# Performance work log

Hardware: AMD Instinct MI355X
Metric: run time of the kernel (lower is better)

The kernel has to match this reference:

```python
import jax, jax.numpy as jnp
import numpy as np

B, S, D, H = 2, 2048, 1024, 16
DQ = D // H
EPS = 1e-5


def setup_inputs() -> dict:
    key = jax.random.key(0)
    ks = jax.random.split(key, 6)
    scale = 0.02
    return {
        "x": jax.random.normal(ks[0], (B, S, D), dtype=jnp.float32),
        "ln_g": jnp.ones((D,), dtype=jnp.float32),
        "ln_b": jnp.zeros((D,), dtype=jnp.float32),
        "Wq": jax.random.normal(ks[1], (D, D), dtype=jnp.float32) * scale,
        "bq": jnp.zeros((D,), dtype=jnp.float32),
        "Wk": jax.random.normal(ks[2], (D, D), dtype=jnp.float32) * scale,
        "bk": jnp.zeros((D,), dtype=jnp.float32),
        "Wv": jax.random.normal(ks[3], (D, D), dtype=jnp.float32) * scale,
        "bv": jnp.zeros((D,), dtype=jnp.float32),
        "Wo": jax.random.normal(ks[4], (D, D), dtype=jnp.float32) * scale,
        "bo": jnp.zeros((D,), dtype=jnp.float32),
    }


def reference(x, ln_g, ln_b, Wq, bq, Wk, bk, Wv, bv, Wo, bo):
    # pre-LayerNorm (torch default eps=1e-5, biased variance)
    mu = jnp.mean(x, axis=-1, keepdims=True)
    var = jnp.mean((x - mu) ** 2, axis=-1, keepdims=True)
    xn = (x - mu) * jax.lax.rsqrt(var + EPS) * ln_g + ln_b

    # QKV projections; weights stored [d_in, d_out]
    q = xn @ Wq + bq  # [B,S,D]
    k = xn @ Wk + bk
    v = xn @ Wv + bv

    # split heads -> [B,H,S,DQ]
    def heads(t):
        return t.reshape(B, S, H, DQ).transpose(0, 2, 1, 3)
    q, k, v = heads(q), heads(k), heads(v)

    scores = jnp.einsum("bhqd,bhkd->bhqk", q, k) / jnp.sqrt(jnp.float32(DQ))
    causal = jnp.tril(jnp.ones((S, S), dtype=bool))  # True = keep
    scores = jnp.where(causal, scores, -jnp.inf)
    probs = jax.nn.softmax(scores, axis=-1)
    attn = jnp.einsum("bhqk,bhkd->bhqd", probs, v)  # [B,H,S,DQ]

    # merge heads: [B,H,S,DQ] -> [B,S,H*DQ] (matches transpose/flatten/transpose)
    merged = attn.transpose(0, 2, 1, 3).reshape(B, S, D)
    out = merged @ Wo + bo
    return out + x
```

## Files before the change

### kernel.cpp

```cpp
#include <hip/hip_runtime.h>
#include <math.h>

#define BB 2
#define SS 2048
#define DD 1024
#define HH 16
#define DQK 64
#define NROWS (BB * SS)
#define NE ((size_t)BB * SS * DD)

using short8 = __attribute__((ext_vector_type(8))) short;
using f32x4  = __attribute__((ext_vector_type(4))) float;

__device__ __forceinline__ ushort f2bf(float f) {
  union { float f; unsigned u; } c; c.f = f;
  return (ushort)((c.u + 0x7fffu + ((c.u >> 16) & 1u)) >> 16);
}

__device__ __forceinline__ unsigned cvt_pk_bf16(float lo, float hi) {
  unsigned r;
  asm("v_cvt_pk_bf16_f32 %0, %1, %2" : "=v"(r) : "v"(lo), "v"(hi));
  return r;
}

__device__ __forceinline__ f32x4 mfma16(short8 a, short8 b, f32x4 c) {
  return __builtin_amdgcn_mfma_f32_16x16x32_bf16(a, b, c, 0, 0, 0);
}

typedef __attribute__((address_space(1))) const unsigned gas_u32;
typedef __attribute__((address_space(3))) unsigned las_u32;
__device__ __forceinline__ void gload_lds16(const void* g, void* l) {
  __builtin_amdgcn_global_load_lds((gas_u32*)g, (las_u32*)l, 16, 0, 0);
}

__global__ __launch_bounds__(256) void prep(const float* __restrict__ x,
                                            const float* __restrict__ g,
                                            const float* __restrict__ bta,
                                            ushort* __restrict__ xn,
                                            const float* __restrict__ Wq,
                                            const float* __restrict__ Wk,
                                            const float* __restrict__ Wv,
                                            const float* __restrict__ Wo,
                                            ushort* __restrict__ wt) {
  __shared__ float tile[64][65];
  const int t = threadIdx.x;
  if (blockIdx.x < NROWS) {
    const int row = blockIdx.x;
    float4 v = ((const float4*)(x + (size_t)row * DD))[t];
    float s  = v.x + v.y + v.z + v.w;
    float ss = v.x * v.x + v.y * v.y + v.z * v.z + v.w * v.w;
#pragma unroll
    for (int off = 32; off > 0; off >>= 1) {
      s  += __shfl_xor(s, off);
      ss += __shfl_xor(ss, off);
    }
    const int wid = t >> 6, lane = t & 63;
    if (lane == 0) { tile[0][wid] = s; tile[0][4 + wid] = ss; }
    __syncthreads();
    const float stot  = tile[0][0] + tile[0][1] + tile[0][2] + tile[0][3];
    const float sstot = tile[0][4] + tile[0][5] + tile[0][6] + tile[0][7];
    const float mu  = stot * (1.0f / DD);
    const float var = sstot * (1.0f / DD) - mu * mu;
    const float inv = rsqrtf(var + 1e-5f);
    const float4 g4 = ((const float4*)g)[t];
    const float4 b4 = ((const float4*)bta)[t];
    ushort4 o;
    o.x = f2bf((v.x - mu) * inv * g4.x + b4.x);
    o.y = f2bf((v.y - mu) * inv * g4.y + b4.y);
    o.z = f2bf((v.z - mu) * inv * g4.z + b4.z);
    o.w = f2bf((v.w - mu) * inv * g4.w + b4.w);
    ((ushort4*)(xn + (size_t)row * DD))[t] = o;
  } else {
    const int wb = blockIdx.x - NROWS;
    const int z = wb >> 8;
    const int k0 = (wb & 15) * 64, n0 = ((wb >> 4) & 15) * 64;
    const float* W = (z == 0) ? Wq : (z == 1) ? Wk : (z == 2) ? Wv : Wo;
    ushort* dst = wt + (size_t)z * DD * DD;
    const int tr = t >> 4, tc = (t & 15) * 4;
#pragma unroll
    for (int rr = 0; rr < 64; rr += 16) {
      float4 v = *(const float4*)(W + (size_t)(k0 + rr + tr) * DD + n0 + tc);
      tile[rr + tr][tc + 0] = v.x;
      tile[rr + tr][tc + 1] = v.y;
      tile[rr + tr][tc + 2] = v.z;
      tile[rr + tr][tc + 3] = v.w;
    }
    __syncthreads();
#pragma unroll
    for (int rr = 0; rr < 64; rr += 16) {
      const int n = rr + tr;
      ushort4 o;
      o.x = f2bf(tile[tc + 0][n]);
      o.y = f2bf(tile[tc + 1][n]);
      o.z = f2bf(tile[tc + 2][n]);
      o.w = f2bf(tile[tc + 3][n]);
      *(ushort4*)(dst + (size_t)(n0 + n) * DD + k0 + tc) = o;
    }
  }
}

#define GEMM_CORE(Ag, Bg)                                                     \
  f32x4 acc[4][4];                                                            \
  _Pragma("unroll")                                                           \
  for (int m = 0; m < 4; ++m)                                                 \
    _Pragma("unroll")                                                         \
    for (int n = 0; n < 4; ++n) acc[m][n] = (f32x4){0.f, 0.f, 0.f, 0.f};     \
  const int cs = ((t & 3) * 16) ^ (((t >> 3) & 3) * 16);                      \
  const int fsw = ((r16 >> 1) & 3) * 16;                                      \
  {                                                                           \
    GSTAGE(Ag, Bg, 0, 0);                                                     \
    GSTAGE(Ag, Bg, 1, 32);                                                    \
    int cb = 0;                                                               \
    for (int k0 = 0; k0 < DD; k0 += 32) {                                     \
      __builtin_amdgcn_sched_barrier(0);                                      \
      if (k0 + 32 < DD) {                                                     \
        asm volatile("s_waitcnt vmcnt(4)" ::: "memory");                      \
      } else {                                                                \
        asm volatile("s_waitcnt vmcnt(0)" ::: "memory");                      \
      }                                                                       \
      __builtin_amdgcn_s_barrier();                                           \
      __builtin_amdgcn_sched_barrier(0);                                      \
      if (k0 + 64 < DD) {                                                     \
        int nb = cb + 2; if (nb >= 3) nb -= 3;                                \
        GSTAGE(Ag, Bg, nb, k0 + 64);                                          \
      }                                                                       \
      const char* Ac = (const char*)&As[cb][0][0];                            \
      const char* Bc = (const char*)&Bs[cb][0][0];                            \
      short8 af[4], bf[4];                                                    \
      _Pragma("unroll")                                                       \
      for (int m = 0; m < 4; ++m)                                             \
        af[m] = *(const short8*)(Ac + (wr * 64 + m * 16 + r16) * 64 +         \
                                 ((g * 16) ^ fsw));                           \
      _Pragma("unroll")                                                       \
      for (int n = 0; n < 4; ++n)                                             \
        bf[n] = *(const short8*)(Bc + (wc * 64 + n * 16 + r16) * 64 +         \
                                 ((g * 16) ^ fsw));                           \
      _Pragma("unroll")                                                       \
      for (int m = 0; m < 4; ++m)                                             \
        _Pragma("unroll")                                                     \
        for (int n = 0; n < 4; ++n) acc[m][n] = mfma16(af[m], bf[n], acc[m][n]); \
      cb = (cb + 1 == 3) ? 0 : cb + 1;                                        \
    }                                                                         \
  }

#define GSTAGE(Ag, Bg, buf, k0)                                               \
  {                                                                           \
    _Pragma("unroll")                                                         \
    for (int i = 0; i < 2; ++i) {                                             \
      gload_lds16(Ag + (size_t)(row0 + i * 64 + (t >> 2)) * (DD * 2) +        \
                      (k0) * 2 + cs,                                          \
                  (char*)&As[buf][0][0] + i * 4096 + t * 16);                 \
      gload_lds16(Bg + (size_t)(col0 + i * 64 + (t >> 2)) * (DD * 2) +        \
                      (k0) * 2 + cs,                                          \
                  (char*)&Bs[buf][0][0] + i * 4096 + t * 16);                 \
    }                                                                         \
  }

__global__ __launch_bounds__(256) void gemm_qkv(
    const ushort* __restrict__ A, const ushort* __restrict__ wt,
    const float* __restrict__ bq, const float* __restrict__ bk,
    const float* __restrict__ bv, ushort* __restrict__ qb,
    ushort* __restrict__ kb, ushort* __restrict__ vt) {
  __shared__ ushort As[3][128][32];
  __shared__ ushort Bs[3][128][32];
  const int t = threadIdx.x;
  const int lane = t & 63;
  const int w = t >> 6, wr = w >> 1, wc = w & 1;
  const int r16 = lane & 15, g = lane >> 4;
  const int row0 = blockIdx.x * 128;
  const int mat = blockIdx.y >> 3;
  const int col0 = (blockIdx.y & 7) * 128;
  const char* Ag = (const char*)A;
  const char* Bg = (const char*)(wt + (size_t)mat * DD * DD);
  const float* bias = (mat == 0) ? bq : (mat == 1) ? bk : bv;
  const float scl = (mat == 0) ? 0.125f * 1.44269504f : 1.0f;

  GEMM_CORE(Ag, Bg)

#pragma unroll
  for (int n = 0; n < 4; ++n) {
    const int c = col0 + wc * 64 + n * 16 + r16;
    const float bc = bias[c];
#pragma unroll
    for (int m = 0; m < 4; ++m) {
      const int rbase = row0 + wr * 64 + m * 16 + g * 4;
      if (mat < 2) {
        ushort* outb = (mat == 0) ? qb : kb;
#pragma unroll
        for (int e = 0; e < 4; ++e)
          outb[(size_t)(rbase + e) * DD + c] = f2bf((acc[m][n][e] + bc) * scl);
      } else {
        uint2 st;
        st.x = cvt_pk_bf16(acc[m][n][0] + bc, acc[m][n][1] + bc);
        st.y = cvt_pk_bf16(acc[m][n][2] + bc, acc[m][n][3] + bc);
        const size_t vrow = (size_t)((rbase >> 11) * HH + (c >> 6)) * DQK + (c & 63);
        *(uint2*)(vt + vrow * SS + (rbase & 2047)) = st;
      }
    }
  }
}

__global__ __launch_bounds__(256) void gemm_o(
    const ushort* __restrict__ A, const ushort* __restrict__ Bt,
    const float* __restrict__ bias, const float* __restrict__ resid,
    float* __restrict__ outf) {
  __shared__ ushort As[3][128][32];
  __shared__ ushort Bs[3][128][32];
  const int t = threadIdx.x;
  const int lane = t & 63;
  const int w = t >> 6, wr = w >> 1, wc = w & 1;
  const int r16 = lane & 15, g = lane >> 4;
  const int row0 = blockIdx.x * 128;
  const int col0 = blockIdx.y * 128;
  const char* Ag = (const char*)A;
  const char* Bg = (const char*)Bt;

  GEMM_CORE(Ag, Bg)

#pragma unroll
  for (int n = 0; n < 4; ++n) {
    const int c = col0 + wc * 64 + n * 16 + r16;
    const float bc = bias[c];
#pragma unroll
    for (int m = 0; m < 4; ++m) {
      const int rbase = row0 + wr * 64 + m * 16 + g * 4;
#pragma unroll
      for (int e = 0; e < 4; ++e) {
        const size_t idx = (size_t)(rbase + e) * DD + c;
        outf[idx] = acc[m][n][e] + bc + resid[idx];
      }
    }
  }
}

__global__ __launch_bounds__(256) void attn_mfma(const ushort* __restrict__ Q,
                                                 const ushort* __restrict__ K,
                                                 const ushort* __restrict__ Vt,
                                                 ushort* __restrict__ O) {
  __shared__ ushort Ks[2][64][64];
  __shared__ ushort Vs[2][64][64];

  const int t = threadIdx.x, lane = t & 63, ww = t >> 6;
  const int r16 = lane & 15, g = lane >> 4;

  const int bid = blockIdx.x;
  const int xcd = bid & 7;
  const int bh = xcd * 4 + ((bid >> 3) & 3);
  const int m = (bid >> 5) & 7;
  const int j = bid >> 8;
  const int qb = (j == 0) ? (31 - m) : (j == 1) ? m : (j == 2) ? (23 - m) : (8 + m);
  const int b = bh >> 4, h = bh & 15;
  const size_t tokbase = (size_t)b * SS;
  const size_t hoff = (size_t)h * DQK;
  const int q0 = qb * 64 + ww * 16;
  const int nt = qb + 1;

  const int srow = t >> 3;
  const int scol = (t & 7) * 16;
  const char* Kb = (const char*)(K + tokbase * DD + hoff);
  const char* Vb = (const char*)(Vt + (size_t)bh * DQK * SS);
  const int sw = ((r16 & 3) | ((r16 >> 1) & 4)) << 4;
  const int rlo = (r16 & 3) + ((r16 >> 2) << 3);

#define STAGE(buf, j0)                                                        \
  {                                                                           \
    _Pragma("unroll")                                                         \
    for (int i = 0; i < 2; ++i) {                                             \
      const int R = i * 32 + srow;                                            \
      const int Cs = scol ^ (((R & 3) | ((R >> 1) & 4)) << 4);                \
      gload_lds16(Kb + ((size_t)((j0) + R) * DD) * 2 + Cs,                    \
                  (char*)&Ks[buf][0][0] + i * 4096 + ww * 1024);              \
      gload_lds16(Vb + ((size_t)R * SS + (j0)) * 2 + Cs,                      \
                  (char*)&Vs[buf][0][0] + i * 4096 + ww * 1024);              \
    }                                                                         \
  }

  short8 qf[2];
#pragma unroll
  for (int kc = 0; kc < 2; ++kc)
    qf[kc] = *(const short8*)(Q + (tokbase + q0 + r16) * DD + hoff + kc * 32 + g * 8);

  f32x4 o[4];
#pragma unroll
  for (int dt = 0; dt < 4; ++dt) o[dt] = (f32x4){0.f, 0.f, 0.f, 0.f};
  float rm = -INFINITY, rl = 0.f;

  STAGE(0, 0);
  int cur = 0;
  for (int tt = 0; tt < nt; ++tt) {
    __builtin_amdgcn_sched_barrier(0);
    asm volatile("s_waitcnt vmcnt(0)" ::: "memory");
    __builtin_amdgcn_s_barrier();
    __builtin_amdgcn_sched_barrier(0);
    if (tt + 1 < nt) STAGE(cur ^ 1, (tt + 1) * 64);

    const char* Kc = (const char*)&Ks[cur][0][0];
    const char* Vc = (const char*)&Vs[cur][0][0];

    f32x4 s4[4];
    __builtin_amdgcn_s_setprio(1);
#pragma unroll
    for (int t2 = 0; t2 < 4; ++t2) {
      const int kk = rlo + (t2 & 1) * 4 + (t2 >> 1) * 32;
      const int sk = ((kk & 3) | ((kk >> 1) & 4)) << 4;
      const int rb = kk * 128;
      const short8 k0 = *(const short8*)(Kc + rb + ((g * 16) ^ sk));
      const short8 k1 = *(const short8*)(Kc + rb + ((64 + g * 16) ^ sk));
      f32x4 s = mfma16(k0, qf[0], (f32x4){0.f, 0.f, 0.f, 0.f});
      s4[t2] = mfma16(k1, qf[1], s);
    }
    __builtin_amdgcn_s_setprio(0);

    if (tt == nt - 1) {
      const int thrl = q0 + r16 - g * 8 - tt * 64;
#pragma unroll
      for (int t2 = 0; t2 < 4; ++t2) {
        const int bb = (t2 & 1) * 4 + (t2 >> 1) * 32;
#pragma unroll
        for (int r = 0; r < 4; ++r)
          s4[t2][r] = (bb + r <= thrl) ? s4[t2][r] : -INFINITY;
      }
    }

    float mx = fmaxf(
        fmaxf(fmaxf(fmaxf(s4[0][0], s4[0][1]), fmaxf(s4[0][2], s4[0][3])),
              fmaxf(fmaxf(s4[1][0], s4[1][1]), fmaxf(s4[1][2], s4[1][3]))),
        fmaxf(fmaxf(fmaxf(s4[2][0], s4[2][1]), fmaxf(s4[2][2], s4[2][3])),
              fmaxf(fmaxf(s4[3][0], s4[3][1]), fmaxf(s4[3][2], s4[3][3]))));

    if (!__all(mx - rm <= 8.f)) {
      float mf = fmaxf(mx, __shfl_xor(mx, 16));
      mf = fmaxf(mf, __shfl_xor(mf, 32));
      const float mn = fmaxf(rm, mf);
      const float sc = __builtin_amdgcn_exp2f(rm - mn);
      rl *= sc;
#pragma unroll
      for (int dt = 0; dt < 4; ++dt) o[dt] *= sc;
      rm = mn;
    }

    union { unsigned u[4]; short8 s; } pbu[2];
#pragma unroll
    for (int t2 = 0; t2 < 4; ++t2) {
      const float p0 = __builtin_amdgcn_exp2f(s4[t2][0] - rm);
      const float p1 = __builtin_amdgcn_exp2f(s4[t2][1] - rm);
      const float p2 = __builtin_amdgcn_exp2f(s4[t2][2] - rm);
      const float p3 = __builtin_amdgcn_exp2f(s4[t2][3] - rm);
      rl += (p0 + p1) + (p2 + p3);
      pbu[t2 >> 1].u[(t2 & 1) * 2 + 0] = cvt_pk_bf16(p0, p1);
      pbu[t2 >> 1].u[(t2 & 1) * 2 + 1] = cvt_pk_bf16(p2, p3);
    }

    __builtin_amdgcn_s_setprio(1);
#pragma unroll
    for (int kc = 0; kc < 2; ++kc) {
#pragma unroll
      for (int dt = 0; dt < 4; ++dt) {
        const short8 vf = *(const short8*)(Vc + (dt * 16 + r16) * 128 +
                                           ((kc * 64 + g * 16) ^ sw));
        o[dt] = mfma16(vf, pbu[kc].s, o[dt]);
      }
    }
    __builtin_amdgcn_s_setprio(0);
    cur ^= 1;
  }
#undef STAGE

  rl += __shfl_xor(rl, 16);
  rl += __shfl_xor(rl, 32);
  const float inv = 1.0f / rl;
#pragma unroll
  for (int dt = 0; dt < 4; ++dt) {
    uint2 st;
    st.x = cvt_pk_bf16(o[dt][0] * inv, o[dt][1] * inv);
    st.y = cvt_pk_bf16(o[dt][2] * inv, o[dt][3] * inv);
    *(uint2*)(O + (tokbase + q0 + r16) * DD + hoff + dt * 16 + g * 4) = st;
  }
}

extern "C" void kernel_launch(void* const* d_in, const int* in_sizes, int n_in,
                              void* d_out, int out_size, void* d_ws, size_t ws_size,
                              hipStream_t stream) {
  const float* x    = (const float*)d_in[0];
  const float* ln_g = (const float*)d_in[1];
  const float* ln_b = (const float*)d_in[2];
  const float* Wq   = (const float*)d_in[3];
  const float* bq   = (const float*)d_in[4];
  const float* Wk   = (const float*)d_in[5];
  const float* bk   = (const float*)d_in[6];
  const float* Wv   = (const float*)d_in[7];
  const float* bv   = (const float*)d_in[8];
  const float* Wo   = (const float*)d_in[9];
  const float* bo   = (const float*)d_in[10];
  float* out = (float*)d_out;

  ushort* ws  = (ushort*)d_ws;
  ushort* xn  = ws;
  ushort* qb  = xn + NE;
  ushort* kb  = qb + NE;
  ushort* vt  = kb + NE;
  ushort* ab  = vt + NE;
  ushort* wt  = ab + NE;
  ushort* wot = wt + (size_t)3 * DD * DD;

  prep<<<NROWS + 1024, 256, 0, stream>>>(x, ln_g, ln_b, xn, Wq, Wk, Wv, Wo, wt);

  gemm_qkv<<<dim3(NROWS / 128, 24), 256, 0, stream>>>(xn, wt, bq, bk, bv,
                                                      qb, kb, vt);

  attn_mfma<<<BB * HH * (SS / 64), 256, 0, stream>>>(qb, kb, vt, ab);

  gemm_o<<<dim3(NROWS / 128, DD / 128), 256, 0, stream>>>(ab, wot, bo, x, out);
}
```

Before: 107.8 us.

## Pair causal q-blocks per attention block with triple-buffered K/V; narrow gemm_o tiles

The attention kernel now has each block process two query tiles (p and 31-p), so every block does 33 K/V iterations and causal work is balanced. It moves from double to triple buffering, with K loads issued separately from V loads and finer vmcnt waits, so QK^T can start before V arrives. The output GEMM drops to 128x64 tiles, doubling the grid for more parallelism at the cost of lower per-block reuse. Costs include more LDS per attention block, half as many attention blocks, and an extra barrier in each iteration.

```diff
diff --git a/kernel.cpp b/kernel.cpp
--- a/kernel.cpp
+++ b/kernel.cpp
@@ -156,6 +156,61 @@
     }                                                                         \
   }
 
+#define GEMM_CORE_O(Ag, Bg)                                                   \
+  f32x4 acc[4][2];                                                            \
+  _Pragma("unroll")                                                           \
+  for (int m = 0; m < 4; ++m)                                                 \
+    _Pragma("unroll")                                                         \
+    for (int n = 0; n < 2; ++n) acc[m][n] = (f32x4){0.f, 0.f, 0.f, 0.f};     \
+  const int cs = ((t & 3) * 16) ^ (((t >> 3) & 3) * 16);                      \
+  const int fsw = ((r16 >> 1) & 3) * 16;                                      \
+  {                                                                           \
+    GSTAGE_O(Ag, Bg, 0, 0);                                                   \
+    GSTAGE_O(Ag, Bg, 1, 32);                                                  \
+    int cb = 0;                                                               \
+    for (int k0 = 0; k0 < DD; k0 += 32) {                                     \
+      __builtin_amdgcn_sched_barrier(0);                                      \
+      if (k0 + 32 < DD) {                                                     \
+        asm volatile("s_waitcnt vmcnt(3)" ::: "memory");                      \
+      } else {                                                                \
+        asm volatile("s_waitcnt vmcnt(0)" ::: "memory");                      \
+      }                                                                       \
+      __builtin_amdgcn_s_barrier();                                           \
+      __builtin_amdgcn_sched_barrier(0);                                      \
+      if (k0 + 64 < DD) {                                                     \
+        int nb = cb + 2; if (nb >= 3) nb -= 3;                                \
+        GSTAGE_O(Ag, Bg, nb, k0 + 64);                                        \
+      }                                                                       \
+      const char* Ac = (const char*)&As[cb][0][0];                            \
+      const char* Bc = (const char*)&Bs[cb][0][0];                            \
+      short8 af[4], bf[2];                                                    \
+      _Pragma("unroll")                                                       \
+      for (int m = 0; m < 4; ++m)                                             \
+        af[m] = *(const short8*)(Ac + (wr * 64 + m * 16 + r16) * 64 +         \
+                                 ((g * 16) ^ fsw));                           \
+      _Pragma("unroll")                                                       \
+      for (int n = 0; n < 2; ++n)                                             \
+        bf[n] = *(const short8*)(Bc + (wc * 32 + n * 16 + r16) * 64 +         \
+                                 ((g * 16) ^ fsw));                           \
+      _Pragma("unroll")                                                       \
+      for (int m = 0; m < 4; ++m)                                             \
+        _Pragma("unroll")                                                     \
+        for (int n = 0; n < 2; ++n) acc[m][n] = mfma16(af[m], bf[n], acc[m][n]); \
+      cb = (cb + 1 == 3) ? 0 : cb + 1;                                        \
+    }                                                                         \
+  }
+
+#define GSTAGE_O(Ag, Bg, buf, k0)                                             \
+  {                                                                           \
+    _Pragma("unroll")                                                         \
+    for (int i = 0; i < 2; ++i)                                               \
+      gload_lds16(Ag + (size_t)(row0 + i * 64 + (t >> 2)) * (DD * 2) +        \
+                      (k0) * 2 + cs,                                          \
+                  (char*)&As[buf][0][0] + i * 4096 + t * 16);                 \
+    gload_lds16(Bg + (size_t)(col0 + (t >> 2)) * (DD * 2) + (k0) * 2 + cs,    \
+                (char*)&Bs[buf][0][0] + t * 16);                              \
+  }
+
 __global__ __launch_bounds__(256) void gemm_qkv(
     const ushort* __restrict__ A, const ushort* __restrict__ wt,
     const float* __restrict__ bq, const float* __restrict__ bk,
@@ -205,21 +260,21 @@
     const float* __restrict__ bias, const float* __restrict__ resid,
     float* __restrict__ outf) {
   __shared__ ushort As[3][128][32];
-  __shared__ ushort Bs[3][128][32];
+  __shared__ ushort Bs[3][64][32];
   const int t = threadIdx.x;
   const int lane = t & 63;
   const int w = t >> 6, wr = w >> 1, wc = w & 1;
   const int r16 = lane & 15, g = lane >> 4;
   const int row0 = blockIdx.x * 128;
-  const int col0 = blockIdx.y * 128;
+  const int col0 = blockIdx.y * 64;
   const char* Ag = (const char*)A;
   const char* Bg = (const char*)Bt;
 
-  GEMM_CORE(Ag, Bg)
-
-#pragma unroll
-  for (int n = 0; n < 4; ++n) {
-    const int c = col0 + wc * 64 + n * 16 + r16;
+  GEMM_CORE_O(Ag, Bg)
+
+#pragma unroll
+  for (int n = 0; n < 2; ++n) {
+    const int c = col0 + wc * 32 + n * 16 + r16;
     const float bc = bias[c];
 #pragma unroll
     for (int m = 0; m < 4; ++m) {
@@ -237,8 +292,8 @@
                                                  const ushort* __restrict__ K,
                                                  const ushort* __restrict__ Vt,
                                                  ushort* __restrict__ O) {
-  __shared__ ushort Ks[2][64][64];
-  __shared__ ushort Vs[2][64][64];
+  __shared__ ushort Ks[3][64][64];
+  __shared__ ushort Vs[3][64][64];
 
   const int t = threadIdx.x, lane = t & 63, ww = t >> 6;
   const int r16 = lane & 15, g = lane >> 4;
@@ -246,14 +301,12 @@
   const int bid = blockIdx.x;
   const int xcd = bid & 7;
   const int bh = xcd * 4 + ((bid >> 3) & 3);
-  const int m = (bid >> 5) & 7;
-  const int j = bid >> 8;
-  const int qb = (j == 0) ? (31 - m) : (j == 1) ? m : (j == 2) ? (23 - m) : (8 + m);
+  const int p = bid >> 5;
+  const int nt1 = 32 - p;
+  const int nt2 = p + 1;
   const int b = bh >> 4, h = bh & 15;
   const size_t tokbase = (size_t)b * SS;
   const size_t hoff = (size_t)h * DQK;
-  const int q0 = qb * 64 + ww * 16;
-  const int nt = qb + 1;
 
   const int srow = t >> 3;
   const int scol = (t & 7) * 16;
@@ -270,15 +323,23 @@
       const int Cs = scol ^ (((R & 3) | ((R >> 1) & 4)) << 4);                \
       gload_lds16(Kb + ((size_t)((j0) + R) * DD) * 2 + Cs,                    \
                   (char*)&Ks[buf][0][0] + i * 4096 + ww * 1024);              \
+    }                                                                         \
+    _Pragma("unroll")                                                         \
+    for (int i = 0; i < 2; ++i) {                                             \
+      const int R = i * 32 + srow;                                            \
+      const int Cs = scol ^ (((R & 3) | ((R >> 1) & 4)) << 4);                \
       gload_lds16(Vb + ((size_t)R * SS + (j0)) * 2 + Cs,                      \
                   (char*)&Vs[buf][0][0] + i * 4096 + ww * 1024);              \
     }                                                                         \
   }
 
-  short8 qf[2];
-#pragma unroll
-  for (int kc = 0; kc < 2; ++kc)
-    qf[kc] = *(const short8*)(Q + (tokbase + q0 + r16) * DD + hoff + kc * 32 + g * 8);
+  int q0 = (31 - p) * 64 + ww * 16;
+  const int q02 = p * 64 + ww * 16;
+  short8 qc0, qc1, q2f0, q2f1;
+  qc0 = *(const short8*)(Q + (tokbase + q0 + r16) * DD + hoff + 0 * 32 + g * 8);
+  qc1 = *(const short8*)(Q + (tokbase + q0 + r16) * DD + hoff + 1 * 32 + g * 8);
+  q2f0 = *(const short8*)(Q + (tokbase + q02 + r16) * DD + hoff + 0 * 32 + g * 8);
+  q2f1 = *(const short8*)(Q + (tokbase + q02 + r16) * DD + hoff + 1 * 32 + g * 8);
 
   f32x4 o[4];
 #pragma unroll
@@ -286,16 +347,42 @@
   float rm = -INFINITY, rl = 0.f;
 
   STAGE(0, 0);
-  int cur = 0;
-  for (int tt = 0; tt < nt; ++tt) {
+  STAGE(1, 64);
+  int cb = 0;
+#pragma unroll 1
+  for (int vt = 0; vt < 33; ++vt) {
+    if (vt == nt1) {
+      float rls = rl;
+      rls += __shfl_xor(rls, 16);
+      rls += __shfl_xor(rls, 32);
+      const float inv = 1.0f / rls;
+#pragma unroll
+      for (int dt = 0; dt < 4; ++dt) {
+        uint2 st;
+        st.x = cvt_pk_bf16(o[dt][0] * inv, o[dt][1] * inv);
+        st.y = cvt_pk_bf16(o[dt][2] * inv, o[dt][3] * inv);
+        *(uint2*)(O + (tokbase + q0 + r16) * DD + hoff + dt * 16 + g * 4) = st;
+        o[dt] = (f32x4){0.f, 0.f, 0.f, 0.f};
+      }
+      rm = -INFINITY; rl = 0.f;
+      q0 = q02; qc0 = q2f0; qc1 = q2f1;
+    }
+
     __builtin_amdgcn_sched_barrier(0);
-    asm volatile("s_waitcnt vmcnt(0)" ::: "memory");
+    asm volatile("s_waitcnt vmcnt(6)" ::: "memory");
     __builtin_amdgcn_s_barrier();
     __builtin_amdgcn_sched_barrier(0);
-    if (tt + 1 < nt) STAGE(cur ^ 1, (tt + 1) * 64);
-
-    const char* Kc = (const char*)&Ks[cur][0][0];
-    const char* Vc = (const char*)&Vs[cur][0][0];
+
+    {
+      const int w2 = vt + 2;
+      int jj = (w2 < nt1) ? w2 : (w2 - nt1);
+      if (w2 >= nt1 && jj >= nt2) jj = 0;
+      int nb = cb + 2; if (nb >= 3) nb -= 3;
+      STAGE(nb, jj * 64);
+    }
+
+    const char* Kc = (const char*)&Ks[cb][0][0];
+    const char* Vc = (const char*)&Vs[cb][0][0];
 
     f32x4 s4[4];
     __builtin_amdgcn_s_setprio(1);
@@ -306,13 +393,15 @@
       const int rb = kk * 128;
       const short8 k0 = *(const short8*)(Kc + rb + ((g * 16) ^ sk));
       const short8 k1 = *(const short8*)(Kc + rb + ((64 + g * 16) ^ sk));
-      f32x4 s = mfma16(k0, qf[0], (f32x4){0.f, 0.f, 0.f, 0.f});
-      s4[t2] = mfma16(k1, qf[1], s);
+      f32x4 s = mfma16(k0, qc0, (f32x4){0.f, 0.f, 0.f, 0.f});
+      s4[t2] = mfma16(k1, qc1, s);
     }
     __builtin_amdgcn_s_setprio(0);
 
-    if (tt == nt - 1) {
-      const int thrl = q0 + r16 - g * 8 - tt * 64;
+    const bool lastseg = (vt == nt1 - 1) || (vt == 32);
+    if (lastseg) {
+      const int tloc = (vt >= nt1) ? (vt - nt1) : vt;
+      const int thrl = q0 + r16 - g * 8 - tloc * 64;
 #pragma unroll
       for (int t2 = 0; t2 < 4; ++t2) {
         const int bb = (t2 & 1) * 4 + (t2 >> 1) * 32;
@@ -351,6 +440,11 @@
       pbu[t2 >> 1].u[(t2 & 1) * 2 + 1] = cvt_pk_bf16(p2, p3);
     }
 
+    __builtin_amdgcn_sched_barrier(0);
+    asm volatile("s_waitcnt vmcnt(8)" ::: "memory");
+    __builtin_amdgcn_s_barrier();
+    __builtin_amdgcn_sched_barrier(0);
+
     __builtin_amdgcn_s_setprio(1);
 #pragma unroll
     for (int kc = 0; kc < 2; ++kc) {
@@ -362,7 +456,7 @@
       }
     }
     __builtin_amdgcn_s_setprio(0);
-    cur ^= 1;
+    cb = (cb + 1 == 3) ? 0 : cb + 1;
   }
 #undef STAGE
 
@@ -408,7 +502,7 @@
   gemm_qkv<<<dim3(NROWS / 128, 24), 256, 0, stream>>>(xn, wt, bq, bk, bv,
                                                       qb, kb, vt);
 
-  attn_mfma<<<BB * HH * (SS / 64), 256, 0, stream>>>(qb, kb, vt, ab);
-
-  gemm_o<<<dim3(NROWS / 128, DD / 128), 256, 0, stream>>>(ab, wot, bo, x, out);
-}
+  attn_mfma<<<BB * HH * (SS / 128), 256, 0, stream>>>(qb, kb, vt, ab);
+
+  gemm_o<<<dim3(NROWS / 128, DD / 64), 256, 0, stream>>>(ab, wot, bo, x, out);
+}
```

Result: no change. 108.6 us (+0.7%).
